# Optimization experiments

Hardware: AMD Instinct MI355X
Metric: run time of the kernel (lower is better)

## Reference

```python
import jax, jax.numpy as jnp
import numpy as np

LAMBDA_N = 0.01
OUTER_LOOP = 2
INNER_LOOP = 50
MAX_DIST = 0.1
LR = 0.2
LR_DECAY = 0.1
ADAGRAD_EPS = 1e-10


def _normalize(x, eps=1e-12):
    # torch F.normalize: x / max(||x||, eps)
    n = jnp.linalg.norm(x, axis=-1, keepdims=True)
    return x / jnp.maximum(n, eps)


def _interp_bary(tri, vw):
    # tri: [b, n, 3, 3] (3 corners x 3 coords), vw: [b, n, 2]
    bary = jnp.concatenate([vw, 1.0 - vw[..., :1] - vw[..., 1:2]], axis=-1)  # [b,n,3]
    return jnp.einsum('bnij,bni->bnj', tri, bary)


def setup_inputs() -> dict:
    key = jax.random.key(0)
    k0, k1, k2, k3, k4 = jax.random.split(key, 5)
    B, Np, Nv, Nf = 1, 8192, 16384, 16384
    query_V = jax.random.uniform(k0, (B, Np, 3), dtype=jnp.float32)
    query_N = _normalize(jax.random.normal(k1, (B, Np, 3), dtype=jnp.float32))
    mesh_V = jax.random.uniform(k2, (Nv, 3), dtype=jnp.float32)
    mesh_F = jax.random.randint(k3, (Nf, 3), 0, Nv, dtype=jnp.int64)
    mesh_N = _normalize(jax.random.normal(k4, (Nv, 3), dtype=jnp.float32))
    return {'query_V': query_V, 'query_N': query_N, 'mesh_V': mesh_V,
            'mesh_F': mesh_F, 'mesh_N': mesh_N}


def reference(query_V, query_N, mesh_V, mesh_F, mesh_N):
    # ---- init_corres_spt: brute-force KNN (K=1) to face centers ----
    F_centers = mesh_V[mesh_F].mean(axis=1)                     # [Nf, 3]
    # squared distances [B, Np, Nf] (pytorch3d knn_points returns squared dist)
    d2 = (jnp.sum(query_V * query_V, axis=-1, keepdims=True)
          - 2.0 * jnp.einsum('bnd,fd->bnf', query_V, F_centers)
          + jnp.sum(F_centers * F_centers, axis=-1))
    spt_fidx = jnp.argmin(d2, axis=-1)                          # [B, Np]
    dmin = jnp.min(d2, axis=-1)
    outlier_mask = dmin > MAX_DIST
    valid = ~outlier_mask
    mask = valid.astype(query_V.dtype)                          # [B, Np]
    denom = jnp.maximum(jnp.sum(mask), 1.0)

    spt_vw0 = jnp.full(query_V.shape[:-1] + (2,), 1.0 / 3.0, dtype=query_V.dtype)

    tri = mesh_F[spt_fidx]          # [B, Np, 3] vertex indices (gather)
    tri_V = mesh_V[tri]             # [B, Np, 3, 3]
    tri_N = mesh_N[tri]             # [B, Np, 3, 3]

    def loss_fn(delta, vw_base):
        vw = vw_base + delta
        corres_V = _interp_bary(tri_V, vw)
        loss_v = jnp.linalg.norm(corres_V - query_V, axis=-1)   # [B, Np]
        corres_N = _normalize(_interp_bary(tri_N, vw))
        loss_n = jnp.linalg.norm(corres_N - query_N, axis=-1)
        per_point = loss_v + LAMBDA_N * loss_n
        # masked mean over valid points only (original indexes out valid points)
        return jnp.sum(per_point * mask) / denom

    grad_fn = jax.grad(loss_fn)

    def solve_delta_vw(vw_base):
        # Adagrad(lr=0.2, lr_decay=0.1), 50 steps
        def step(carry, i):
            delta, ssum = carry
            g = grad_fn(delta, vw_base)
            ssum = ssum + g * g
            clr = LR / (1.0 + i * LR_DECAY)
            delta = delta - clr * g / (jnp.sqrt(ssum) + ADAGRAD_EPS)
            return (delta, ssum), None
        z = jnp.zeros_like(vw_base)
        (delta, _), _ = jax.lax.scan(step, (z, z),
                                     jnp.arange(INNER_LOOP, dtype=vw_base.dtype))
        return delta

    # ---- update_corres_spt: outer loop with alpha halving ----
    vw = spt_vw0
    alpha = 1.0
    for _ in range(OUTER_LOOP):
        delta = solve_delta_vw(vw)
        vw = vw + delta * alpha       # triwalk fallback: spt_vw + spt_delta
        alpha = alpha * 0.5

    # invalid (outlier) points keep their init barycentric coords
    spt_vw = jnp.where(valid[..., None], vw, spt_vw0)
    return spt_fidx, spt_vw, outlier_mask
```

## Files before the change

### kernel.cpp

```cpp
#include <hip/hip_runtime.h>
#include <math.h>

#define NP 8192
#define NF 16384
#define GQ 16

__global__ __launch_bounds__(256) void k_centers(const float* __restrict__ mV,
                                                 const int* __restrict__ mF,
                                                 double* __restrict__ ctr,
                                                 double* __restrict__ clrtab) {
    if (blockIdx.x == 0 && threadIdx.x < 50) {
        clrtab[threadIdx.x] = 0.2 / (1.0 + (double)threadIdx.x * 0.1);
    }
    int f = blockIdx.x * 256 + threadIdx.x;
    if (f >= NF) return;
    int i0 = mF[3*f+0], i1 = mF[3*f+1], i2 = mF[3*f+2];
    double cx = ((double)mV[3*i0+0] + (double)mV[3*i1+0] + (double)mV[3*i2+0]) / 3.0;
    double cy = ((double)mV[3*i0+1] + (double)mV[3*i1+1] + (double)mV[3*i2+1]) / 3.0;
    double cz = ((double)mV[3*i0+2] + (double)mV[3*i1+2] + (double)mV[3*i2+2]) / 3.0;
    ctr[4*f+0] = cx; ctr[4*f+1] = cy; ctr[4*f+2] = cz;
    ctr[4*f+3] = cx*cx + cy*cy + cz*cz;
}

__global__ __launch_bounds__(256) void k_knn(const float* __restrict__ qV,
                                             const double* __restrict__ ctr,
                                             float* __restrict__ out,
                                             int* __restrict__ fidx_ws,
                                             int* __restrict__ valid_ws) {
    int pbase = blockIdx.x * GQ;
    double qx[GQ], qy[GQ], qz[GQ];
    #pragma unroll
    for (int g = 0; g < GQ; ++g) {
        int p = pbase + g;
        qx[g] = (double)qV[3*p+0];
        qy[g] = (double)qV[3*p+1];
        qz[g] = (double)qV[3*p+2];
    }
    double best[GQ]; int bidx[GQ];
    #pragma unroll
    for (int g = 0; g < GQ; ++g) { best[g] = 1e300; bidx[g] = 0x7fffffff; }

    const double4* ctr4 = (const double4*)ctr;
    #pragma unroll 2
    for (int f = threadIdx.x; f < NF; f += 256) {
        double4 c = ctr4[f];
        #pragma unroll
        for (int g = 0; g < GQ; ++g) {
            double dot = qx[g]*c.x + qy[g]*c.y + qz[g]*c.z;
            double key = c.w - 2.0*dot;
            if (key < best[g]) { best[g] = key; bidx[g] = f; }
        }
    }
    #pragma unroll
    for (int off = 32; off > 0; off >>= 1) {
        #pragma unroll
        for (int g = 0; g < GQ; ++g) {
            double ov = __shfl_down(best[g], off);
            int    oi = __shfl_down(bidx[g], off);
            if (ov < best[g] || (ov == best[g] && oi < bidx[g])) { best[g] = ov; bidx[g] = oi; }
        }
    }
    __shared__ double sv[4][GQ];
    __shared__ int    si[4][GQ];
    int wid = threadIdx.x >> 6, lane = threadIdx.x & 63;
    if (lane == 0) {
        #pragma unroll
        for (int g = 0; g < GQ; ++g) { sv[wid][g] = best[g]; si[wid][g] = bidx[g]; }
    }
    __syncthreads();
    if (threadIdx.x == 0) {
        for (int g = 0; g < GQ; ++g) {
            double bv = sv[0][g]; int bi = si[0][g];
            for (int w2 = 1; w2 < 4; ++w2) {
                double ov = sv[w2][g]; int oi = si[w2][g];
                if (ov < bv || (ov == bv && oi < bi)) { bv = ov; bi = oi; }
            }
            int p = pbase + g;
            double4 c = ctr4[bi];
            double dot = qx[g]*c.x + qy[g]*c.y + qz[g]*c.z;
            double qq  = qx[g]*qx[g] + qy[g]*qy[g] + qz[g]*qz[g];
            double d2  = (qq - 2.0*dot) + c.w;
            int outlier = (d2 > 0.1) ? 1 : 0;
            fidx_ws[p]  = bi;
            valid_ws[p] = 1 - outlier;
            out[p]          = (float)bi;
            out[3*NP + p]   = outlier ? 1.0f : 0.0f;
        }
    }
}

__global__ __launch_bounds__(256) void k_denom(const int* __restrict__ valid_ws,
                                               double* __restrict__ denom) {
    __shared__ int s[256];
    int acc = 0;
    for (int i = threadIdx.x; i < NP; i += 256) acc += valid_ws[i];
    s[threadIdx.x] = acc;
    __syncthreads();
    for (int off = 128; off > 0; off >>= 1) {
        if (threadIdx.x < off) s[threadIdx.x] += s[threadIdx.x + off];
        __syncthreads();
    }
    if (threadIdx.x == 0) {
        double d = (double)s[0];
        denom[0] = d > 1.0 ? d : 1.0;
    }
}

__global__ __launch_bounds__(256) void k_opt(const float* __restrict__ qV,
                                             const float* __restrict__ qN,
                                             const float* __restrict__ mV,
                                             const int* __restrict__ mF,
                                             const float* __restrict__ mN,
                                             const int* __restrict__ fidx_ws,
                                             const int* __restrict__ valid_ws,
                                             const double* __restrict__ denomp,
                                             const double* __restrict__ clrtab,
                                             float* __restrict__ out) {
    int p = blockIdx.x * 256 + threadIdx.x;
    if (p >= NP) return;
    const float third = (float)(1.0/3.0);
    if (!valid_ws[p]) {
        out[NP + 2*p + 0] = third;
        out[NP + 2*p + 1] = third;
        return;
    }
    double inv_denom = 1.0 / denomp[0];
    int f = fidx_ws[p];
    int i0 = mF[3*f+0], i1 = mF[3*f+1], i2 = mF[3*f+2];

    double V0x = mV[3*i0+0], V0y = mV[3*i0+1], V0z = mV[3*i0+2];
    double V1x = mV[3*i1+0], V1y = mV[3*i1+1], V1z = mV[3*i1+2];
    double V2x = mV[3*i2+0], V2y = mV[3*i2+1], V2z = mV[3*i2+2];
    double N0x = mN[3*i0+0], N0y = mN[3*i0+1], N0z = mN[3*i0+2];
    double N1x = mN[3*i1+0], N1y = mN[3*i1+1], N1z = mN[3*i1+2];
    double N2x = mN[3*i2+0], N2y = mN[3*i2+1], N2z = mN[3*i2+2];
    double qx  = qV[3*p+0],  qy  = qV[3*p+1],  qz  = qV[3*p+2];
    double qnx = qN[3*p+0],  qny = qN[3*p+1],  qnz = qN[3*p+2];

    double Eux = V0x - V2x, Euy = V0y - V2y, Euz = V0z - V2z;
    double Ewx = V1x - V2x, Ewy = V1y - V2y, Ewz = V1z - V2z;
    double Fux = N0x - N2x, Fuy = N0y - N2y, Fuz = N0z - N2z;
    double Fwx = N1x - N2x, Fwy = N1y - N2y, Fwz = N1z - N2z;
    double Kx  = V2x - qx,  Ky  = V2y - qy,  Kz  = V2z - qz;

    double u = 1.0/3.0, w = 1.0/3.0;
    double alpha = 1.0;
    for (int outer = 0; outer < 2; ++outer) {
        double du = 0.0, dw = 0.0, su = 0.0, sw = 0.0;
        for (int it = 0; it < 50; ++it) {
            double uu = u + du, ww = w + dw;
            double rvx = uu*Eux + ww*Ewx + Kx;
            double rvy = uu*Euy + ww*Ewy + Ky;
            double rvz = uu*Euz + ww*Ewz + Kz;
            double L2v = rvx*rvx + rvy*rvy + rvz*rvz;
            double invLv = rsqrt(L2v);
            double gu = (rvx*Eux + rvy*Euy + rvz*Euz) * invLv;
            double gw = (rvx*Ewx + rvy*Ewy + rvz*Ewz) * invLv;
            double nx = uu*Fux + ww*Fwx + N2x;
            double ny = uu*Fuy + ww*Fwy + N2y;
            double nz = uu*Fuz + ww*Fwz + N2z;
            double m2 = nx*nx + ny*ny + nz*nz;
            bool   mok = (m2 > 1e-24);
            double inv = mok ? rsqrt(m2) : 1e12;
            double hx = nx*inv, hy = ny*inv, hz = nz*inv;
            double rnx = hx - qnx, rny = hy - qny, rnz = hz - qnz;
            double L2n = rnx*rnx + rny*rny + rnz*rnz;
            double invLn = rsqrt(L2n);
            double A_u = rnx*Fux + rny*Fuy + rnz*Fuz;
            double A_w = rnx*Fwx + rny*Fwy + rnz*Fwz;
            double B   = rnx*nx + rny*ny + rnz*nz;
            double C_u = nx*Fux + ny*Fuy + nz*Fuz;
            double C_w = nx*Fwx + ny*Fwy + nz*Fwz;
            double s = mok ? ((B*inv)*inv)*inv : 0.0;
            double gnu = (A_u*inv - s*C_u) * invLn;
            double gnw = (A_w*inv - s*C_w) * invLn;
            gu = (gu + 0.01*gnu) * inv_denom;
            gw = (gw + 0.01*gnw) * inv_denom;
            su += gu*gu; sw += gw*gw;
            double clr = clrtab[it];
            du -= clr * gu / (sqrt(su) + 1e-10);
            dw -= clr * gw / (sqrt(sw) + 1e-10);
        }
        u += du * alpha; w += dw * alpha;
        alpha *= 0.5;
    }
    out[NP + 2*p + 0] = (float)u;
    out[NP + 2*p + 1] = (float)w;
}

extern "C" void kernel_launch(void* const* d_in, const int* in_sizes, int n_in,
                              void* d_out, int out_size, void* d_ws, size_t ws_size,
                              hipStream_t stream) {
    const float* qV = (const float*)d_in[0];
    const float* qN = (const float*)d_in[1];
    const float* mV = (const float*)d_in[2];
    const int*   mF = (const int*)d_in[3];
    const float* mN = (const float*)d_in[4];
    float* out = (float*)d_out;

    double* ctr      = (double*)d_ws;
    double* denom    = ctr + (size_t)NF*4;
    double* clrtab   = denom + 1;
    int*    fidx_ws  = (int*)(clrtab + 50);
    int*    valid_ws = fidx_ws + NP;

    hipLaunchKernelGGL(k_centers, dim3(NF/256), dim3(256), 0, stream, mV, mF, ctr, clrtab);
    hipLaunchKernelGGL(k_knn,     dim3(NP/GQ),  dim3(256), 0, stream, qV, ctr, out, fidx_ws, valid_ws);
    hipLaunchKernelGGL(k_denom,   dim3(1),      dim3(256), 0, stream, valid_ws, denom);
    hipLaunchKernelGGL(k_opt,     dim3(NP/256), dim3(256), 0, stream,
                       qV, qN, mV, mF, mN, fidx_ws, valid_ws, denom, clrtab, out);
}
```

Before: 106.6 us.

## Split KNN face range across blocks with separate reduction kernel

The brute-force nearest-center search now splits the face list into four chunks. Each block handles one query group and one chunk, writing partial minima to workspace, and a new reduce kernel merges the four partials per point and computes the outlier flag. This raises the block count from 512 to 2048, so the fp64 distance loop can fill more of the GPU's compute units. In exchange it adds an extra kernel launch, partial-result traffic, and repeated query loads and shuffle reductions per chunk.

```diff
diff --git a/kernel.cpp b/kernel.cpp
--- a/kernel.cpp
+++ b/kernel.cpp
@@ -4,6 +4,9 @@
 #define NP 8192
 #define NF 16384
 #define GQ 16
+#define SPLIT 4
+#define NFS (NF / SPLIT)
+#define NG (NP / GQ)
 
 __global__ __launch_bounds__(256) void k_centers(const float* __restrict__ mV,
                                                  const int* __restrict__ mF,
@@ -22,42 +25,46 @@
     ctr[4*f+3] = cx*cx + cy*cy + cz*cz;
 }
 
-__global__ __launch_bounds__(256) void k_knn(const float* __restrict__ qV,
-                                             const double* __restrict__ ctr,
-                                             float* __restrict__ out,
-                                             int* __restrict__ fidx_ws,
-                                             int* __restrict__ valid_ws) {
-    int pbase = blockIdx.x * GQ;
+__global__ __launch_bounds__(256) void k_knn_part(const float* __restrict__ qV,
+                                                  const double* __restrict__ ctr,
+                                                  double* __restrict__ pkey,
+                                                  int* __restrict__ pidx) {
+    int g = blockIdx.x / SPLIT;
+    int s = blockIdx.x % SPLIT;
+    int pbase = g * GQ;
+    int fbase = s * NFS;
+
     double qx[GQ], qy[GQ], qz[GQ];
     #pragma unroll
-    for (int g = 0; g < GQ; ++g) {
-        int p = pbase + g;
-        qx[g] = (double)qV[3*p+0];
-        qy[g] = (double)qV[3*p+1];
-        qz[g] = (double)qV[3*p+2];
+    for (int gg = 0; gg < GQ; ++gg) {
+        int p = pbase + gg;
+        qx[gg] = (double)qV[3*p+0];
+        qy[gg] = (double)qV[3*p+1];
+        qz[gg] = (double)qV[3*p+2];
     }
     double best[GQ]; int bidx[GQ];
     #pragma unroll
-    for (int g = 0; g < GQ; ++g) { best[g] = 1e300; bidx[g] = 0x7fffffff; }
+    for (int gg = 0; gg < GQ; ++gg) { best[gg] = 1e300; bidx[gg] = 0x7fffffff; }
 
     const double4* ctr4 = (const double4*)ctr;
     #pragma unroll 2
-    for (int f = threadIdx.x; f < NF; f += 256) {
+    for (int fo = threadIdx.x; fo < NFS; fo += 256) {
+        int f = fbase + fo;
         double4 c = ctr4[f];
         #pragma unroll
-        for (int g = 0; g < GQ; ++g) {
-            double dot = qx[g]*c.x + qy[g]*c.y + qz[g]*c.z;
+        for (int gg = 0; gg < GQ; ++gg) {
+            double dot = qx[gg]*c.x + qy[gg]*c.y + qz[gg]*c.z;
             double key = c.w - 2.0*dot;
-            if (key < best[g]) { best[g] = key; bidx[g] = f; }
+            if (key < best[gg]) { best[gg] = key; bidx[gg] = f; }
         }
     }
     #pragma unroll
     for (int off = 32; off > 0; off >>= 1) {
         #pragma unroll
-        for (int g = 0; g < GQ; ++g) {
-            double ov = __shfl_down(best[g], off);
-            int    oi = __shfl_down(bidx[g], off);
-            if (ov < best[g] || (ov == best[g] && oi < bidx[g])) { best[g] = ov; bidx[g] = oi; }
+        for (int gg = 0; gg < GQ; ++gg) {
+            double ov = __shfl_down(best[gg], off);
+            int    oi = __shfl_down(bidx[gg], off);
+            if (ov < best[gg] || (ov == best[gg] && oi < bidx[gg])) { best[gg] = ov; bidx[gg] = oi; }
         }
     }
     __shared__ double sv[4][GQ];
@@ -65,28 +72,51 @@
     int wid = threadIdx.x >> 6, lane = threadIdx.x & 63;
     if (lane == 0) {
         #pragma unroll
-        for (int g = 0; g < GQ; ++g) { sv[wid][g] = best[g]; si[wid][g] = bidx[g]; }
+        for (int gg = 0; gg < GQ; ++gg) { sv[wid][gg] = best[gg]; si[wid][gg] = bidx[gg]; }
     }
     __syncthreads();
     if (threadIdx.x == 0) {
-        for (int g = 0; g < GQ; ++g) {
-            double bv = sv[0][g]; int bi = si[0][g];
+        for (int gg = 0; gg < GQ; ++gg) {
+            double bv = sv[0][gg]; int bi = si[0][gg];
             for (int w2 = 1; w2 < 4; ++w2) {
-                double ov = sv[w2][g]; int oi = si[w2][g];
+                double ov = sv[w2][gg]; int oi = si[w2][gg];
                 if (ov < bv || (ov == bv && oi < bi)) { bv = ov; bi = oi; }
             }
-            int p = pbase + g;
-            double4 c = ctr4[bi];
-            double dot = qx[g]*c.x + qy[g]*c.y + qz[g]*c.z;
-            double qq  = qx[g]*qx[g] + qy[g]*qy[g] + qz[g]*qz[g];
-            double d2  = (qq - 2.0*dot) + c.w;
-            int outlier = (d2 > 0.1) ? 1 : 0;
-            fidx_ws[p]  = bi;
-            valid_ws[p] = 1 - outlier;
-            out[p]          = (float)bi;
-            out[3*NP + p]   = outlier ? 1.0f : 0.0f;
-        }
-    }
+            int slot = (g * SPLIT + s) * GQ + gg;
+            pkey[slot] = bv;
+            pidx[slot] = bi;
+        }
+    }
+}
+
+__global__ __launch_bounds__(256) void k_knn_reduce(const float* __restrict__ qV,
+                                                    const double* __restrict__ ctr,
+                                                    const double* __restrict__ pkey,
+                                                    const int* __restrict__ pidx,
+                                                    float* __restrict__ out,
+                                                    int* __restrict__ fidx_ws,
+                                                    int* __restrict__ valid_ws) {
+    int p = blockIdx.x * 256 + threadIdx.x;
+    if (p >= NP) return;
+    int g = p / GQ, j = p % GQ;
+    double bv = 1e300; int bi = 0x7fffffff;
+    #pragma unroll
+    for (int s = 0; s < SPLIT; ++s) {
+        int slot = (g * SPLIT + s) * GQ + j;
+        double ov = pkey[slot]; int oi = pidx[slot];
+        if (ov < bv || (ov == bv && oi < bi)) { bv = ov; bi = oi; }
+    }
+    const double4* ctr4 = (const double4*)ctr;
+    double4 c = ctr4[bi];
+    double qx = (double)qV[3*p+0], qy = (double)qV[3*p+1], qz = (double)qV[3*p+2];
+    double dot = qx*c.x + qy*c.y + qz*c.z;
+    double qq  = qx*qx + qy*qy + qz*qz;
+    double d2  = (qq - 2.0*dot) + c.w;
+    int outlier = (d2 > 0.1) ? 1 : 0;
+    fidx_ws[p]  = bi;
+    valid_ws[p] = 1 - outlier;
+    out[p]        = (float)bi;
+    out[3*NP + p] = outlier ? 1.0f : 0.0f;
 }
 
 __global__ __launch_bounds__(256) void k_denom(const int* __restrict__ valid_ws,
@@ -201,12 +231,16 @@
     double* ctr      = (double*)d_ws;
     double* denom    = ctr + (size_t)NF*4;
     double* clrtab   = denom + 1;
-    int*    fidx_ws  = (int*)(clrtab + 50);
+    double* pkey     = clrtab + 50;
+    int*    pidx     = (int*)(pkey + (size_t)NG*SPLIT*GQ);
+    int*    fidx_ws  = pidx + (size_t)NG*SPLIT*GQ;
     int*    valid_ws = fidx_ws + NP;
 
-    hipLaunchKernelGGL(k_centers, dim3(NF/256), dim3(256), 0, stream, mV, mF, ctr, clrtab);
-    hipLaunchKernelGGL(k_knn,     dim3(NP/GQ),  dim3(256), 0, stream, qV, ctr, out, fidx_ws, valid_ws);
-    hipLaunchKernelGGL(k_denom,   dim3(1),      dim3(256), 0, stream, valid_ws, denom);
-    hipLaunchKernelGGL(k_opt,     dim3(NP/256), dim3(256), 0, stream,
+    hipLaunchKernelGGL(k_centers,    dim3(NF/256),   dim3(256), 0, stream, mV, mF, ctr, clrtab);
+    hipLaunchKernelGGL(k_knn_part,   dim3(NG*SPLIT), dim3(256), 0, stream, qV, ctr, pkey, pidx);
+    hipLaunchKernelGGL(k_knn_reduce, dim3(NP/256),   dim3(256), 0, stream, qV, ctr, pkey, pidx,
+                       out, fidx_ws, valid_ws);
+    hipLaunchKernelGGL(k_denom,      dim3(1),        dim3(256), 0, stream, valid_ws, denom);
+    hipLaunchKernelGGL(k_opt,        dim3(NP/256),   dim3(256), 0, stream,
                        qV, qN, mV, mF, mN, fidx_ws, valid_ws, denom, clrtab, out);
 }
```

Result: slower. 141.4 us (+32.7%).

## Run KNN search in fp32 with top-2 margin check and fp64 repair pass

Applied to the files above, without the earlier changes.

The brute-force nearest-face search now runs in single precision on a float4 copy of the face centers. It tracks the best and second-best keys per query, and flags queries whose gap falls below a small margin. A new kernel launched over every point redoes the search in double precision for the flagged points only, so the result stays exact. This removes most of the fp64 arithmetic from the dominant search loop. In exchange it adds an extra launch of 8192 blocks that mostly exit early, plus more per-element compare logic; the queries per block also drop from 16 to 8.

```diff
diff --git a/kernel.cpp b/kernel.cpp
--- a/kernel.cpp
+++ b/kernel.cpp
@@ -3,11 +3,13 @@
 
 #define NP 8192
 #define NF 16384
-#define GQ 16
+#define GQ 8
+#define MARGIN 1e-5f
 
 __global__ __launch_bounds__(256) void k_centers(const float* __restrict__ mV,
                                                  const int* __restrict__ mF,
                                                  double* __restrict__ ctr,
+                                                 float4* __restrict__ ctrf,
                                                  double* __restrict__ clrtab) {
     if (blockIdx.x == 0 && threadIdx.x < 50) {
         clrtab[threadIdx.x] = 0.2 / (1.0 + (double)threadIdx.x * 0.1);
@@ -18,74 +20,141 @@
     double cx = ((double)mV[3*i0+0] + (double)mV[3*i1+0] + (double)mV[3*i2+0]) / 3.0;
     double cy = ((double)mV[3*i0+1] + (double)mV[3*i1+1] + (double)mV[3*i2+1]) / 3.0;
     double cz = ((double)mV[3*i0+2] + (double)mV[3*i1+2] + (double)mV[3*i2+2]) / 3.0;
-    ctr[4*f+0] = cx; ctr[4*f+1] = cy; ctr[4*f+2] = cz;
-    ctr[4*f+3] = cx*cx + cy*cy + cz*cz;
+    double cc = cx*cx + cy*cy + cz*cz;
+    ctr[4*f+0] = cx; ctr[4*f+1] = cy; ctr[4*f+2] = cz; ctr[4*f+3] = cc;
+    ctrf[f] = make_float4((float)cx, (float)cy, (float)cz, (float)cc);
 }
 
 __global__ __launch_bounds__(256) void k_knn(const float* __restrict__ qV,
+                                             const float4* __restrict__ ctrf,
                                              const double* __restrict__ ctr,
                                              float* __restrict__ out,
                                              int* __restrict__ fidx_ws,
-                                             int* __restrict__ valid_ws) {
+                                             int* __restrict__ valid_ws,
+                                             int* __restrict__ flag) {
     int pbase = blockIdx.x * GQ;
-    double qx[GQ], qy[GQ], qz[GQ];
+    float qx[GQ], qy[GQ], qz[GQ];
     #pragma unroll
     for (int g = 0; g < GQ; ++g) {
         int p = pbase + g;
-        qx[g] = (double)qV[3*p+0];
-        qy[g] = (double)qV[3*p+1];
-        qz[g] = (double)qV[3*p+2];
-    }
-    double best[GQ]; int bidx[GQ];
-    #pragma unroll
-    for (int g = 0; g < GQ; ++g) { best[g] = 1e300; bidx[g] = 0x7fffffff; }
-
-    const double4* ctr4 = (const double4*)ctr;
+        qx[g] = qV[3*p+0];
+        qy[g] = qV[3*p+1];
+        qz[g] = qV[3*p+2];
+    }
+    float b1[GQ], b2[GQ]; int i1[GQ];
+    #pragma unroll
+    for (int g = 0; g < GQ; ++g) { b1[g] = 1e30f; b2[g] = 1e30f; i1[g] = 0x7fffffff; }
+
     #pragma unroll 2
     for (int f = threadIdx.x; f < NF; f += 256) {
-        double4 c = ctr4[f];
+        float4 c = ctrf[f];
         #pragma unroll
         for (int g = 0; g < GQ; ++g) {
-            double dot = qx[g]*c.x + qy[g]*c.y + qz[g]*c.z;
-            double key = c.w - 2.0*dot;
-            if (key < best[g]) { best[g] = key; bidx[g] = f; }
+            float dot = qx[g]*c.x + qy[g]*c.y + qz[g]*c.z;
+            float key = c.w - 2.0f*dot;
+            float ob1 = b1[g];
+            bool lt = key < ob1;
+            b1[g] = lt ? key : ob1;
+            i1[g] = lt ? f : i1[g];
+            float cand2 = lt ? ob1 : key;
+            b2[g] = cand2 < b2[g] ? cand2 : b2[g];
         }
     }
     #pragma unroll
     for (int off = 32; off > 0; off >>= 1) {
         #pragma unroll
         for (int g = 0; g < GQ; ++g) {
-            double ov = __shfl_down(best[g], off);
-            int    oi = __shfl_down(bidx[g], off);
-            if (ov < best[g] || (ov == best[g] && oi < bidx[g])) { best[g] = ov; bidx[g] = oi; }
-        }
-    }
-    __shared__ double sv[4][GQ];
-    __shared__ int    si[4][GQ];
+            float ob1 = __shfl_down(b1[g], off);
+            int   oi1 = __shfl_down(i1[g], off);
+            float ob2 = __shfl_down(b2[g], off);
+            bool win = (ob1 < b1[g]) || (ob1 == b1[g] && oi1 < i1[g]);
+            float loser = win ? b1[g] : ob1;
+            b1[g] = win ? ob1 : b1[g];
+            i1[g] = win ? oi1 : i1[g];
+            float mb2 = ob2 < b2[g] ? ob2 : b2[g];
+            b2[g] = loser < mb2 ? loser : mb2;
+        }
+    }
+    __shared__ float sv1[4][GQ], sv2[4][GQ];
+    __shared__ int   si1[4][GQ];
     int wid = threadIdx.x >> 6, lane = threadIdx.x & 63;
     if (lane == 0) {
         #pragma unroll
-        for (int g = 0; g < GQ; ++g) { sv[wid][g] = best[g]; si[wid][g] = bidx[g]; }
+        for (int g = 0; g < GQ; ++g) { sv1[wid][g] = b1[g]; si1[wid][g] = i1[g]; sv2[wid][g] = b2[g]; }
     }
     __syncthreads();
     if (threadIdx.x == 0) {
+        const double4* ctr4 = (const double4*)ctr;
         for (int g = 0; g < GQ; ++g) {
-            double bv = sv[0][g]; int bi = si[0][g];
+            float bv = sv1[0][g], r2 = sv2[0][g]; int bi = si1[0][g];
             for (int w2 = 1; w2 < 4; ++w2) {
-                double ov = sv[w2][g]; int oi = si[w2][g];
-                if (ov < bv || (ov == bv && oi < bi)) { bv = ov; bi = oi; }
+                float ob1 = sv1[w2][g], ob2 = sv2[w2][g]; int oi1 = si1[w2][g];
+                bool win = (ob1 < bv) || (ob1 == bv && oi1 < bi);
+                float loser = win ? bv : ob1;
+                bv = win ? ob1 : bv;
+                bi = win ? oi1 : bi;
+                float mb2 = ob2 < r2 ? ob2 : r2;
+                r2 = loser < mb2 ? loser : mb2;
             }
             int p = pbase + g;
+            flag[p] = (r2 - bv < MARGIN) ? 1 : 0;
             double4 c = ctr4[bi];
-            double dot = qx[g]*c.x + qy[g]*c.y + qz[g]*c.z;
-            double qq  = qx[g]*qx[g] + qy[g]*qy[g] + qz[g]*qz[g];
+            double dqx = (double)qx[g], dqy = (double)qy[g], dqz = (double)qz[g];
+            double dot = dqx*c.x + dqy*c.y + dqz*c.z;
+            double qq  = dqx*dqx + dqy*dqy + dqz*dqz;
             double d2  = (qq - 2.0*dot) + c.w;
             int outlier = (d2 > 0.1) ? 1 : 0;
             fidx_ws[p]  = bi;
             valid_ws[p] = 1 - outlier;
-            out[p]          = (float)bi;
-            out[3*NP + p]   = outlier ? 1.0f : 0.0f;
-        }
+            out[p]        = (float)bi;
+            out[3*NP + p] = outlier ? 1.0f : 0.0f;
+        }
+    }
+}
+
+__global__ __launch_bounds__(256) void k_repair(const float* __restrict__ qV,
+                                                const double* __restrict__ ctr,
+                                                const int* __restrict__ flag,
+                                                float* __restrict__ out,
+                                                int* __restrict__ fidx_ws,
+                                                int* __restrict__ valid_ws) {
+    int p = blockIdx.x;
+    if (!flag[p]) return;
+    double qx = (double)qV[3*p+0], qy = (double)qV[3*p+1], qz = (double)qV[3*p+2];
+    double best = 1e300; int bidx = 0x7fffffff;
+    const double4* ctr4 = (const double4*)ctr;
+    for (int f = threadIdx.x; f < NF; f += 256) {
+        double4 c = ctr4[f];
+        double dot = qx*c.x + qy*c.y + qz*c.z;
+        double key = c.w - 2.0*dot;
+        if (key < best) { best = key; bidx = f; }
+    }
+    #pragma unroll
+    for (int off = 32; off > 0; off >>= 1) {
+        double ov = __shfl_down(best, off);
+        int    oi = __shfl_down(bidx, off);
+        if (ov < best || (ov == best && oi < bidx)) { best = ov; bidx = oi; }
+    }
+    __shared__ double sv[4];
+    __shared__ int    si[4];
+    int wid = threadIdx.x >> 6, lane = threadIdx.x & 63;
+    if (lane == 0) { sv[wid] = best; si[wid] = bidx; }
+    __syncthreads();
+    if (threadIdx.x == 0) {
+        double bv = sv[0]; int bi = si[0];
+        for (int w2 = 1; w2 < 4; ++w2) {
+            double ov = sv[w2]; int oi = si[w2];
+            if (ov < bv || (ov == bv && oi < bi)) { bv = ov; bi = oi; }
+        }
+        double4 c = ctr4[bi];
+        double dot = qx*c.x + qy*c.y + qz*c.z;
+        double qq  = qx*qx + qy*qy + qz*qz;
+        double d2  = (qq - 2.0*dot) + c.w;
+        int outlier = (d2 > 0.1) ? 1 : 0;
+        fidx_ws[p]  = bi;
+        valid_ws[p] = 1 - outlier;
+        out[p]        = (float)bi;
+        out[3*NP + p] = outlier ? 1.0f : 0.0f;
     }
 }
 
@@ -201,11 +270,16 @@
     double* ctr      = (double*)d_ws;
     double* denom    = ctr + (size_t)NF*4;
     double* clrtab   = denom + 1;
-    int*    fidx_ws  = (int*)(clrtab + 50);
+    float4* ctrf     = (float4*)(clrtab + 50);
+    int*    flag     = (int*)(ctrf + NF);
+    int*    fidx_ws  = flag + NP;
     int*    valid_ws = fidx_ws + NP;
 
-    hipLaunchKernelGGL(k_centers, dim3(NF/256), dim3(256), 0, stream, mV, mF, ctr, clrtab);
-    hipLaunchKernelGGL(k_knn,     dim3(NP/GQ),  dim3(256), 0, stream, qV, ctr, out, fidx_ws, valid_ws);
+    hipLaunchKernelGGL(k_centers, dim3(NF/256), dim3(256), 0, stream, mV, mF, ctr, ctrf, clrtab);
+    hipLaunchKernelGGL(k_knn,     dim3(NP/GQ),  dim3(256), 0, stream, qV, ctrf, ctr,
+                       out, fidx_ws, valid_ws, flag);
+    hipLaunchKernelGGL(k_repair,  dim3(NP),     dim3(256), 0, stream, qV, ctr, flag,
+                       out, fidx_ws, valid_ws);
     hipLaunchKernelGGL(k_denom,   dim3(1),      dim3(256), 0, stream, valid_ws, denom);
     hipLaunchKernelGGL(k_opt,     dim3(NP/256), dim3(256), 0, stream,
                        qV, qN, mV, mF, mN, fidx_ws, valid_ws, denom, clrtab, out);
```

After: 121.8 us. +14.3%, slower.
